# Kernel tuning notes

Hardware: AMD Instinct MI355X
Metric: run time of the kernel (lower is better)

The kernel has to match this reference:

```python
import jax, jax.numpy as jnp
import numpy as np

B, T, E = 4, 2048, 512
H, D = 8, 64            # num_heads, head_size = E // H
HID = H * E             # FFN hidden = num_heads * n_embed (per source)
EPS = 1e-5


def layer_norm(x, g, b):
    mu = jnp.mean(x, axis=-1, keepdims=True)
    var = jnp.var(x, axis=-1, keepdims=True)
    return (x - mu) * jax.lax.rsqrt(var + EPS) * g + b


def setup_inputs() -> dict:
    key = jax.random.key(0)
    ks = jax.random.split(key, 12)
    s_e = 1.0 / np.sqrt(E)
    s_hd = 1.0 / np.sqrt(H * D)
    s_hid = 1.0 / np.sqrt(HID)
    return {
        "x": jax.random.normal(ks[0], (B, T, E), jnp.float32),
        "Wq": jax.random.normal(ks[1], (H, E, D), jnp.float32) * s_e,
        "Wk": jax.random.normal(ks[2], (H, E, D), jnp.float32) * s_e,
        "Wv": jax.random.normal(ks[3], (H, E, D), jnp.float32) * s_e,
        "Wo": jax.random.normal(ks[4], (H * D, E), jnp.float32) * s_hd,
        "bo": jnp.zeros((E,), jnp.float32),
        "W1": jax.random.normal(ks[5], (E, HID), jnp.float32) * s_e,
        "b1": jnp.zeros((HID,), jnp.float32),
        "W2": jax.random.normal(ks[6], (HID, E), jnp.float32) * s_hid,
        "b2": jnp.zeros((E,), jnp.float32),
        "g1": jnp.ones((E,), jnp.float32),
        "be1": jnp.zeros((E,), jnp.float32),
        "g2": jnp.ones((E,), jnp.float32),
        "be2": jnp.zeros((E,), jnp.float32),
    }


def reference(x, Wq, Wk, Wv, Wo, bo, W1, b1, W2, b2, g1, be1, g2, be2):
    # pre-LN decoder block (layer_norm_first=True path)
    xn = layer_norm(x, g1, be1)

    # multi-head causal attention; NOTE: scale is T**-0.5 per the source code
    q = jnp.einsum('bte,hed->bhtd', xn, Wq)
    k = jnp.einsum('bte,hed->bhtd', xn, Wk)
    v = jnp.einsum('bte,hed->bhtd', xn, Wv)
    scores = jnp.einsum('bhtd,bhsd->bhts', q, k) * (T ** -0.5)
    causal = jnp.tril(jnp.ones((T, T), bool))
    scores = jnp.where(causal, scores, -jnp.inf)
    attn = jax.nn.softmax(scores, axis=-1)
    o = jnp.einsum('bhts,bhsd->bhtd', attn, v)           # [B,H,T,D]
    o = o.transpose(0, 2, 1, 3).reshape(B, T, H * D)      # concat heads
    mha = o @ Wo + bo

    x = xn + mha
    xn2 = layer_norm(x, g2, be2)
    ffn = jax.nn.relu(xn2 @ W1 + b1) @ W2 + b2
    return xn2 + ffn
```

## Files before the change

### kernel.cpp

```cpp
#include <hip/hip_runtime.h>
#include <hip/hip_bf16.h>
#include <math.h>

#define Bsz 4
#define Tt 2048
#define Ee 512
#define Hh 8
#define Dd 64
#define HIDs 4096
#define Mrows (Bsz * Tt)

typedef __attribute__((ext_vector_type(8))) short short8;
typedef __attribute__((ext_vector_type(4))) float f32x4;
typedef __attribute__((ext_vector_type(16))) float f32x16;

#define AS1 __attribute__((address_space(1)))
#define AS3 __attribute__((address_space(3)))

__device__ __forceinline__ unsigned short f2bfu(float f) {
    unsigned u = __float_as_uint(f);
    return (unsigned short)((u + 0x7fffu + ((u >> 16) & 1u)) >> 16);
}
__device__ __forceinline__ unsigned short truncbf(float f) {
    return (unsigned short)(__float_as_uint(f) >> 16);
}

__device__ __forceinline__ void ln_body(const float* __restrict__ x,
        const float* __restrict__ g, const float* __restrict__ b,
        const float* __restrict__ addb,
        float* __restrict__ out_f, __hip_bfloat16* __restrict__ out_bf,
        int row) {
    int tid = threadIdx.x;
    const float* xr = x + (size_t)row * Ee;
    float v0 = xr[tid];
    float v1 = xr[tid + 256];
    float s = v0 + v1;
    float sq = v0 * v0 + v1 * v1;
#pragma unroll
    for (int off = 32; off > 0; off >>= 1) {
        s  += __shfl_xor(s, off, 64);
        sq += __shfl_xor(sq, off, 64);
    }
    __shared__ float ls[4], lq[4];
    int wid = tid >> 6, lane = tid & 63;
    if (lane == 0) { ls[wid] = s; lq[wid] = sq; }
    __syncthreads();
    s  = ls[0] + ls[1] + ls[2] + ls[3];
    sq = lq[0] + lq[1] + lq[2] + lq[3];
    float mean = s * (1.0f / Ee);
    float var  = sq * (1.0f / Ee) - mean * mean;
    float rstd = rsqrtf(var + 1e-5f);
    float o0 = (v0 - mean) * rstd * g[tid]       + b[tid];
    float o1 = (v1 - mean) * rstd * g[tid + 256] + b[tid + 256];
    float* orow = out_f + (size_t)row * Ee;
    orow[tid]       = o0 + addb[tid];
    orow[tid + 256] = o1 + addb[tid + 256];
    __hip_bfloat16* brow = out_bf + (size_t)row * Ee;
    brow[tid]       = __float2bfloat16(o0);
    brow[tid + 256] = __float2bfloat16(o1);
}

__global__ __launch_bounds__(256) void ln_kernel(const float* __restrict__ x,
        const float* __restrict__ g, const float* __restrict__ b,
        const float* __restrict__ addb,
        float* __restrict__ out_f, __hip_bfloat16* __restrict__ out_bf) {
    ln_body(x, g, b, addb, out_f, out_bf, blockIdx.x);
}

__device__ __forceinline__ void tr_tile(const float* __restrict__ in,
        __hip_bfloat16* __restrict__ outp, int R, int C, int c0, int r0) {
    __shared__ float tile[64][65];
    int tc = threadIdx.x & 63, tg = threadIdx.x >> 6;
#pragma unroll
    for (int i = 0; i < 16; ++i) {
        int r = tg * 16 + i;
        tile[r][tc] = in[(size_t)(r0 + r) * C + c0 + tc];
    }
    __syncthreads();
#pragma unroll
    for (int i = 0; i < 16; ++i) {
        int cc = tg * 16 + i;
        outp[(size_t)(c0 + cc) * R + r0 + tc] = __float2bfloat16(tile[tc][cc]);
    }
}
__global__ __launch_bounds__(256) void startup_kernel(
        const float* __restrict__ x, const float* __restrict__ g1,
        const float* __restrict__ be1, const float* __restrict__ bo,
        float* __restrict__ xn, __hip_bfloat16* __restrict__ xn_bf,
        const float* __restrict__ Wq, const float* __restrict__ Wk,
        const float* __restrict__ Wv, const float* __restrict__ Wo,
        const float* __restrict__ W1, const float* __restrict__ W2,
        __hip_bfloat16* __restrict__ bqT, __hip_bfloat16* __restrict__ woT,
        __hip_bfloat16* __restrict__ w1T, __hip_bfloat16* __restrict__ w2T) {
    if (blockIdx.x < Mrows) {
        ln_body(x, g1, be1, bo, xn, xn_bf, blockIdx.x);
        return;
    }
    int blk = blockIdx.x - Mrows;
    if (blk < 192) {
        int p = blk >> 6, h = (blk >> 3) & 7, et = blk & 7;
        const float* W = (p == 0) ? Wq : ((p == 1) ? Wk : Wv);
        float sc = (p == 0) ? 0.022097086912079608f * 1.4426950408889634f : 1.0f;
        __shared__ float tile[64][65];
        int td = threadIdx.x & 63, tg = threadIdx.x >> 6;
#pragma unroll
        for (int i = 0; i < 16; ++i) {
            int e = tg * 16 + i;
            tile[e][td] = W[((size_t)h * Ee + et * 64 + e) * Dd + td] * sc;
        }
        __syncthreads();
#pragma unroll
        for (int i = 0; i < 16; ++i) {
            int d = tg * 16 + i;
            bqT[((size_t)(p * 512 + h * 64 + d)) * Ee + et * 64 + td] =
                __float2bfloat16(tile[td][d]);
        }
    } else if (blk < 256) {
        int t = blk - 192;
        tr_tile(Wo, woT, 512, 512, (t & 7) * 64, (t >> 3) * 64);
    } else if (blk < 768) {
        int t = blk - 256;
        tr_tile(W1, w1T, 512, HIDs, (t & 63) * 64, (t >> 6) * 64);
    } else {
        int t = blk - 768;
        tr_tile(W2, w2T, HIDs, 512, (t & 7) * 64, (t >> 3) * 64);
    }
}

__global__ __launch_bounds__(256) void mfma_gemm(
        const __hip_bfloat16* __restrict__ A, int lda,
        const __hip_bfloat16* __restrict__ B, int ldb,
        __hip_bfloat16* __restrict__ Cb, int ldc, int K, int nx) {
    __shared__ __hip_bfloat16 S[16384];
    __hip_bfloat16* As = S;
    __hip_bfloat16* Bs = S + 8192;
    int tid = threadIdx.x;
    int lane = tid & 63, wave = tid >> 6;
    int wm = wave >> 1, wn = wave & 1;
    int L = blockIdx.x;
    int slots = (int)gridDim.x >> 3;
    int v = (L & 7) * slots + (L >> 3);
    int bx = v % nx, by = v / nx;
    int row0 = by * 128, col0 = bx * 128;
    f32x4 acc[4][4];
#pragma unroll
    for (int i = 0; i < 4; ++i)
#pragma unroll
        for (int j = 0; j < 4; ++j) acc[i][j] = (f32x4){0.f, 0.f, 0.f, 0.f};

    int fr = lane & 15;
    int kq = (lane >> 4) << 3;

    for (int k0 = 0; k0 < K; k0 += 64) {
        __syncthreads();
#pragma unroll
        for (int j = 0; j < 4; ++j) {
            int c  = j * 256 + tid;
            int cb = j * 256 + wave * 64;
            int p  = c >> 9, cp = c & 511;
            int r  = cp >> 2, kg = (cp & 3) << 3;
            int ko = k0 + p * 32 + kg;
            __builtin_amdgcn_global_load_lds(
                (const AS1 void*)(A + (size_t)(row0 + r) * lda + ko),
                (AS3 void*)(As + cb * 8), 16, 0, 0);
            __builtin_amdgcn_global_load_lds(
                (const AS1 void*)(B + (size_t)(col0 + r) * ldb + ko),
                (AS3 void*)(Bs + cb * 8), 16, 0, 0);
        }
        __syncthreads();
#pragma unroll
        for (int ks = 0; ks < 2; ++ks) {
            short8 afr[4], bfr[4];
#pragma unroll
            for (int i = 0; i < 4; ++i) {
                afr[i] = *(const short8*)(As + ks * 4096 + (wm * 64 + i * 16 + fr) * 32 + kq);
                bfr[i] = *(const short8*)(Bs + ks * 4096 + (wn * 64 + i * 16 + fr) * 32 + kq);
            }
#pragma unroll
            for (int i = 0; i < 4; ++i)
#pragma unroll
                for (int j = 0; j < 4; ++j)
                    acc[i][j] = __builtin_amdgcn_mfma_f32_16x16x32_bf16(afr[i], bfr[j], acc[i][j], 0, 0, 0);
        }
    }
    __syncthreads();
    unsigned short* Ew = (unsigned short*)S + wave * 1152;
    const __hip_bfloat16* Er = (const __hip_bfloat16*)Ew;
    int rq = (lane >> 4) << 2;
    int rr = lane >> 2, cb2 = (lane & 3) * 16;
#pragma unroll
    for (int i = 0; i < 4; ++i) {
#pragma unroll
        for (int j = 0; j < 4; ++j)
#pragma unroll
            for (int gi = 0; gi < 4; ++gi)
                Ew[(rq + gi) * 72 + j * 16 + fr] = f2bfu(acc[i][j][gi]);
        uint4 v0 = *(const uint4*)(Er + rr * 72 + cb2);
        uint4 v1 = *(const uint4*)(Er + rr * 72 + cb2 + 8);
        size_t rg = (size_t)(row0 + wm * 64 + i * 16 + rr) * ldc + col0 + wn * 64 + cb2;
        *(uint4*)(Cb + rg)     = v0;
        *(uint4*)(Cb + rg + 8) = v1;
    }
}

__global__ __launch_bounds__(256) void mfma_gemm_n64(
        const __hip_bfloat16* __restrict__ A, int lda,
        const __hip_bfloat16* __restrict__ B, int ldb,
        float* __restrict__ Cf, int ldc, int K, int nx) {
    __shared__ __hip_bfloat16 As[2 * 128 * 32];
    __shared__ __hip_bfloat16 Bs[2 * 64 * 32];
    int tid = threadIdx.x;
    int lane = tid & 63, wave = tid >> 6;
    int L = blockIdx.x;
    int slots = (int)gridDim.x >> 3;
    int v = (L & 7) * slots + (L >> 3);
    int bx = v % nx, by = v / nx;
    int row0 = by * 128, col0 = bx * 64;
    f32x4 acc[2][4];
#pragma unroll
    for (int i = 0; i < 2; ++i)
#pragma unroll
        for (int j = 0; j < 4; ++j) acc[i][j] = (f32x4){0.f, 0.f, 0.f, 0.f};

    int fr = lane & 15;
    int kq = (lane >> 4) << 3;

    for (int k0 = 0; k0 < K; k0 += 64) {
        __syncthreads();
#pragma unroll
        for (int j = 0; j < 4; ++j) {
            int c  = j * 256 + tid;
            int cb = j * 256 + wave * 64;
            int p  = c >> 9, cp = c & 511;
            int r  = cp >> 2, kg = (cp & 3) << 3;
            __builtin_amdgcn_global_load_lds(
                (const AS1 void*)(A + (size_t)(row0 + r) * lda + k0 + p * 32 + kg),
                (AS3 void*)(As + cb * 8), 16, 0, 0);
        }
#pragma unroll
        for (int j = 0; j < 2; ++j) {
            int c  = j * 256 + tid;
            int cb = j * 256 + wave * 64;
            int p  = c >> 8, cp = c & 255;
            int r  = cp >> 2, kg = (cp & 3) << 3;
            __builtin_amdgcn_global_load_lds(
                (const AS1 void*)(B + (size_t)(col0 + r) * ldb + k0 + p * 32 + kg),
                (AS3 void*)(Bs + cb * 8), 16, 0, 0);
        }
        __syncthreads();
#pragma unroll
        for (int ks = 0; ks < 2; ++ks) {
            short8 afr[2], bfr[4];
#pragma unroll
            for (int i = 0; i < 2; ++i)
                afr[i] = *(const short8*)(As + ks * 4096 + (wave * 32 + i * 16 + fr) * 32 + kq);
#pragma unroll
            for (int j = 0; j < 4; ++j)
                bfr[j] = *(const short8*)(Bs + ks * 2048 + (j * 16 + fr) * 32 + kq);
#pragma unroll
            for (int i = 0; i < 2; ++i)
#pragma unroll
                for (int j = 0; j < 4; ++j)
                    acc[i][j] = __builtin_amdgcn_mfma_f32_16x16x32_bf16(afr[i], bfr[j], acc[i][j], 0, 0, 0);
        }
    }
    int rq = (lane >> 4) << 2;
#pragma unroll
    for (int i = 0; i < 2; ++i)
#pragma unroll
        for (int j = 0; j < 4; ++j)
#pragma unroll
            for (int gidx = 0; gidx < 4; ++gidx) {
                int r = row0 + wave * 32 + i * 16 + rq + gidx;
                int c = col0 + j * 16 + fr;
                Cf[(size_t)r * ldc + c] += acc[i][j][gidx];
            }
}

__global__ __launch_bounds__(256) void mfma_gemm256(
        const __hip_bfloat16* __restrict__ A, int lda,
        const __hip_bfloat16* __restrict__ B, int ldb,
        __hip_bfloat16* __restrict__ Cb, int ldc, int K,
        const float* __restrict__ bias) {
    __shared__ __hip_bfloat16 S[24576];
    __hip_bfloat16* As = S;
    __hip_bfloat16* Bs = S + 16384;
    int tid = threadIdx.x;
    int lane = tid & 63, wave = tid >> 6;
    int L = blockIdx.x;
    int k8 = L & 7, sub = L >> 3;
    int sr = k8 >> 1, sc = k8 & 1;
    int by = sr * 8 + (sub >> 4);
    int bx = sc * 16 + (sub & 15);
    int row0 = by * 256, col0 = bx * 128;
    f32x4 acc[4][8];
#pragma unroll
    for (int i = 0; i < 4; ++i)
#pragma unroll
        for (int j = 0; j < 8; ++j) acc[i][j] = (f32x4){0.f, 0.f, 0.f, 0.f};

    int fr = lane & 15;
    int kq = (lane >> 4) << 3;
    int nsteps = K >> 5;

#define STAGE256(st, buf)                                                     \
    do {                                                                      \
        int ko_ = (st) << 5;                                                  \
        _Pragma("unroll")                                                     \
        for (int j = 0; j < 4; ++j) {                                         \
            int c = j * 256 + tid;                                            \
            int cb = j * 256 + wave * 64;                                     \
            int r = c >> 2, kg = (c & 3) << 3;                                \
            __builtin_amdgcn_global_load_lds(                                 \
                (const AS1 void*)(A + (size_t)(row0 + r) * lda + ko_ + kg),   \
                (AS3 void*)(As + (buf) * 8192 + cb * 8), 16, 0, 0);           \
        }                                                                     \
        _Pragma("unroll")                                                     \
        for (int j = 0; j < 2; ++j) {                                         \
            int c = j * 256 + tid;                                            \
            int cb = j * 256 + wave * 64;                                     \
            int r = c >> 2, kg = (c & 3) << 3;                                \
            __builtin_amdgcn_global_load_lds(                                 \
                (const AS1 void*)(B + (size_t)(col0 + r) * ldb + ko_ + kg),   \
                (AS3 void*)(Bs + (buf) * 4096 + cb * 8), 16, 0, 0);           \
        }                                                                     \
    } while (0)

    STAGE256(0, 0);
    __syncthreads();
    for (int st = 0; st < nsteps; ++st) {
        int buf = st & 1;
        if (st + 1 < nsteps) STAGE256(st + 1, buf ^ 1);
        short8 afr[4], bfr[8];
#pragma unroll
        for (int i = 0; i < 4; ++i)
            afr[i] = *(const short8*)(As + buf * 8192 + (wave * 64 + i * 16 + fr) * 32 + kq);
#pragma unroll
        for (int j = 0; j < 8; ++j)
            bfr[j] = *(const short8*)(Bs + buf * 4096 + (j * 16 + fr) * 32 + kq);
#pragma unroll
        for (int i = 0; i < 4; ++i)
#pragma unroll
            for (int j = 0; j < 8; ++j)
                acc[i][j] = __builtin_amdgcn_mfma_f32_16x16x32_bf16(afr[i], bfr[j], acc[i][j], 0, 0, 0);
        __syncthreads();
    }
#undef STAGE256

    float bv[8];
#pragma unroll
    for (int j = 0; j < 8; ++j) bv[j] = bias[col0 + j * 16 + fr];
    unsigned short* Ew = (unsigned short*)S + wave * 2176;
    const __hip_bfloat16* Er = (const __hip_bfloat16*)Ew;
    int rq = (lane >> 4) << 2;
    int rr = lane >> 2, cb2 = (lane & 3) * 32;
#pragma unroll
    for (int i = 0; i < 4; ++i) {
#pragma unroll
        for (int j = 0; j < 8; ++j)
#pragma unroll
            for (int gi = 0; gi < 4; ++gi) {
                float t = acc[i][j][gi] + bv[j];
                Ew[(rq + gi) * 136 + j * 16 + fr] = f2bfu(t > 0.f ? t : 0.f);
            }
        size_t rg = (size_t)(row0 + wave * 64 + i * 16 + rr) * ldc + col0 + cb2;
#pragma unroll
        for (int u = 0; u < 4; ++u)
            *(uint4*)(Cb + rg + u * 8) = *(const uint4*)(Er + rr * 136 + cb2 + u * 8);
    }
}

__global__ __launch_bounds__(256) void attn_mfma(const __hip_bfloat16* __restrict__ qkvb,
        __hip_bfloat16* __restrict__ ob) {
    __shared__ __hip_bfloat16 KsS[2][64 * 72];
    __shared__ __hip_bfloat16 VtS[2][64 * 72];
    __shared__ __hip_bfloat16 PsS[4 * 32 * 72];
    __hip_bfloat16* Qs = PsS;

    const unsigned short* q16 = (const unsigned short*)qkvb;
    int tid  = threadIdx.x;
    int lane = tid & 63, wave = tid >> 6;
    int l31 = lane & 31, l5 = lane >> 5;
    int blk = blockIdx.x;
    int qb  = 15 - (blk >> 5);
    int bh  = blk & 31;
    int b = bh >> 3, h = bh & 7;
    int base = qb * 128;
    size_t tokbase = (size_t)b * Tt;
    int qoff = h * 64, koff = 512 + h * 64, voff = 1024 + h * 64;

    {
        int q = tid >> 1, dg = (tid & 1) * 32;
        const unsigned short* src = q16 + (tokbase + base + q) * 1536 + qoff + dg;
        uint4 a  = *(const uint4*)src;
        uint4 b4 = *(const uint4*)(src + 8);
        uint4 c4 = *(const uint4*)(src + 16);
        uint4 d4 = *(const uint4*)(src + 24);
        *(uint4*)(Qs + q * 72 + dg)      = a;
        *(uint4*)(Qs + q * 72 + dg + 8)  = b4;
        *(uint4*)(Qs + q * 72 + dg + 16) = c4;
        *(uint4*)(Qs + q * 72 + dg + 24) = d4;
    }
    __syncthreads();
    short8 aq[4];
#pragma unroll
    for (int kd = 0; kd < 4; ++kd)
        aq[kd] = *(const short8*)(Qs + (wave * 32 + l31) * 72 + kd * 16 + l5 * 8);

    short8 ones;
#pragma unroll
    for (int i = 0; i < 8; ++i) ones[i] = (short)0x3F80;

    f32x16 acc[2], accL;
#pragma unroll
    for (int i = 0; i < 16; ++i) { acc[0][i] = 0.f; acc[1][i] = 0.f; accL[i] = 0.f; }
    __hip_bfloat16* Psw = PsS + wave * (32 * 72);
    unsigned short* Psw16 = (unsigned short*)Psw;

    int s_k = tid >> 2, dg_k = (tid & 3) * 16;
    int sp = (tid & 31) * 2, dg8 = (tid >> 5) * 8;
    uint4 kr0, kr1, va, vb;
    {
        const unsigned short* kp = q16 + (tokbase + s_k) * 1536 + koff + dg_k;
        kr0 = *(const uint4*)kp;
        kr1 = *(const uint4*)(kp + 8);
        const unsigned short* vp = q16 + (tokbase + sp) * 1536 + voff + dg8;
        va = *(const uint4*)vp;
        vb = *(const uint4*)(vp + 1536);
    }

    int tmax = 2 * qb + 1;
    for (int tile = 0; tile <= tmax; ++tile) {
        int buf = tile & 1;
        *(uint4*)(KsS[buf] + s_k * 72 + dg_k)     = kr0;
        *(uint4*)(KsS[buf] + s_k * 72 + dg_k + 8) = kr1;
        {
            unsigned a0[4] = {va.x, va.y, va.z, va.w};
            unsigned b0[4] = {vb.x, vb.y, vb.z, vb.w};
#pragma unroll
            for (int i = 0; i < 4; ++i) {
                unsigned p0 = (a0[i] & 0xffffu) | (b0[i] << 16);
                unsigned p1 = (a0[i] >> 16) | (b0[i] & 0xffff0000u);
                *(unsigned*)(VtS[buf] + (dg8 + 2 * i) * 72 + sp)     = p0;
                *(unsigned*)(VtS[buf] + (dg8 + 2 * i + 1) * 72 + sp) = p1;
            }
        }
        __syncthreads();
        if (tile < tmax) {
            int s1 = (tile + 1) * 64;
            const unsigned short* kp = q16 + (tokbase + s1 + s_k) * 1536 + koff + dg_k;
            kr0 = *(const uint4*)kp;
            kr1 = *(const uint4*)(kp + 8);
            const unsigned short* vp = q16 + (tokbase + s1 + sp) * 1536 + voff + dg8;
            va = *(const uint4*)vp;
            vb = *(const uint4*)(vp + 1536);
        }
        if (tile == tmax && wave < 2) continue;
        f32x16 Sc[2];
#pragma unroll
        for (int i = 0; i < 16; ++i) { Sc[0][i] = 0.f; Sc[1][i] = 0.f; }
#pragma unroll
        for (int st = 0; st < 2; ++st)
#pragma unroll
            for (int kd = 0; kd < 4; ++kd) {
                short8 bk = *(const short8*)(KsS[buf] + (st * 32 + l31) * 72 + kd * 16 + l5 * 8);
                Sc[st] = __builtin_amdgcn_mfma_f32_32x32x16_bf16(aq[kd], bk, Sc[st], 0, 0, 0);
            }
        if (tile >= 2 * qb) {
            int s0t = tile * 64;
            int qrb = base + wave * 32 + 4 * l5;
#pragma unroll
            for (int st = 0; st < 2; ++st) {
                int sg = s0t + st * 32 + l31;
#pragma unroll
                for (int reg = 0; reg < 16; ++reg) {
                    int qr = qrb + (reg & 3) + 8 * (reg >> 2);
                    if (sg > qr) Sc[st][reg] = -1e30f;
                }
            }
        }
#pragma unroll
        for (int st = 0; st < 2; ++st)
#pragma unroll
            for (int reg = 0; reg < 16; ++reg) {
                int pr = (reg & 3) + 8 * (reg >> 2) + 4 * l5;
                Psw16[pr * 72 + st * 32 + l31] =
                    truncbf(__builtin_amdgcn_exp2f(Sc[st][reg]));
            }
#pragma unroll
        for (int ks = 0; ks < 4; ++ks) {
            short8 ap = *(const short8*)(Psw + l31 * 72 + ks * 16 + l5 * 8);
            accL = __builtin_amdgcn_mfma_f32_32x32x16_bf16(ap, ones, accL, 0, 0, 0);
#pragma unroll
            for (int dt = 0; dt < 2; ++dt) {
                short8 bv = *(const short8*)(VtS[buf] + (dt * 32 + l31) * 72 + ks * 16 + l5 * 8);
                acc[dt] = __builtin_amdgcn_mfma_f32_32x32x16_bf16(ap, bv, acc[dt], 0, 0, 0);
            }
        }
    }
#pragma unroll
    for (int reg = 0; reg < 16; ++reg) {
        float rl = 1.0f / accL[reg];
        int qr = base + wave * 32 + (reg & 3) + 8 * (reg >> 2) + 4 * l5;
#pragma unroll
        for (int dt = 0; dt < 2; ++dt)
            ob[(tokbase + qr) * 512 + h * 64 + dt * 32 + l31] =
                __float2bfloat16(acc[dt][reg] * rl);
    }
}

extern "C" void kernel_launch(void* const* d_in, const int* in_sizes, int n_in,
                              void* d_out, int out_size, void* d_ws, size_t ws_size,
                              hipStream_t stream) {
    const float* x   = (const float*)d_in[0];
    const float* Wq  = (const float*)d_in[1];
    const float* Wk  = (const float*)d_in[2];
    const float* Wv  = (const float*)d_in[3];
    const float* Wo  = (const float*)d_in[4];
    const float* bo  = (const float*)d_in[5];
    const float* W1  = (const float*)d_in[6];
    const float* b1  = (const float*)d_in[7];
    const float* W2  = (const float*)d_in[8];
    const float* b2  = (const float*)d_in[9];
    const float* g1  = (const float*)d_in[10];
    const float* be1 = (const float*)d_in[11];
    const float* g2  = (const float*)d_in[12];
    const float* be2 = (const float*)d_in[13];
    float* out = (float*)d_out;

    char* ws = (char*)d_ws;
    __hip_bfloat16* bqT    = (__hip_bfloat16*)(ws);
    __hip_bfloat16* woT    = (__hip_bfloat16*)(ws + 1572864);
    __hip_bfloat16* w1T    = (__hip_bfloat16*)(ws + 2097152);
    __hip_bfloat16* w2T    = (__hip_bfloat16*)(ws + 6291456);
    float*          xn     = (float*)(ws + 10485760);
    __hip_bfloat16* xn_bf  = (__hip_bfloat16*)(ws + 27262976);
    __hip_bfloat16* qkv_bf = (__hip_bfloat16*)(ws + 35651584);
    __hip_bfloat16* o_bf   = (__hip_bfloat16*)(ws + 60817408);
    __hip_bfloat16* h_bf   = (__hip_bfloat16*)(ws + 35651584);

    startup_kernel<<<Mrows + 1280, 256, 0, stream>>>(
        x, g1, be1, bo, xn, xn_bf, Wq, Wk, Wv, Wo, W1, W2, bqT, woT, w1T, w2T);
    mfma_gemm<<<768, 256, 0, stream>>>(
        xn_bf, 512, bqT, 512, qkv_bf, 1536, 512, 12);
    attn_mfma<<<Bsz * Hh * (Tt / 128), 256, 0, stream>>>(qkv_bf, o_bf);
    mfma_gemm_n64<<<512, 256, 0, stream>>>(
        o_bf, 512, woT, 512, xn, 512, 512, 8);
    ln_kernel<<<Mrows, 256, 0, stream>>>(xn, g2, be2, b2, out, xn_bf);
    mfma_gemm256<<<1024, 256, 0, stream>>>(
        xn_bf, 512, w1T, 512, h_bf, HIDs, 512, b1);
    mfma_gemm_n64<<<512, 256, 0, stream>>>(
        h_bf, HIDs, w2T, HIDs, out, 512, HIDs, 8);
}
```

Measured before the change: 340.7 us.

## Rewrite FFN1 GEMM as 256x256 tile, 8-wave, four-phase pipelined kernel

Replaces the 256x128 FFN up-projection GEMM with a 256x256 tile kernel using 512 threads (8 waves in a 2x4 layout), a K-step of 64 and XOR-swizzled LDS to avoid bank conflicts. Each K iteration is split into four quarter-phases, with loads for the next tile issued between barriers, explicit vmcnt waits and raised wave priority around the MFMA bursts. The grid is remapped across 8 XCD-interleaved slots. It uses 128KB of LDS and many accumulator registers, which limits occupancy, and the hand-written waitcnt and barrier schedule is fragile.

```diff
diff --git a/kernel.cpp b/kernel.cpp
--- a/kernel.cpp
+++ b/kernel.cpp
@@ -277,96 +277,196 @@
             }
 }
 
-__global__ __launch_bounds__(256) void mfma_gemm256(
+__device__ __forceinline__ short8 ld_frag(const __hip_bfloat16* base, int r, int slot) {
+    return *(const short8*)(base + r * 64 + ((slot ^ (r & 7)) << 3));
+}
+
+__global__ __launch_bounds__(512, 2) void gemm256_8ph(
         const __hip_bfloat16* __restrict__ A, int lda,
         const __hip_bfloat16* __restrict__ B, int ldb,
         __hip_bfloat16* __restrict__ Cb, int ldc, int K,
-        const float* __restrict__ bias) {
-    __shared__ __hip_bfloat16 S[24576];
-    __hip_bfloat16* As = S;
-    __hip_bfloat16* Bs = S + 16384;
+        const float* __restrict__ bias, int nx) {
+    __shared__ __hip_bfloat16 S[65536];
+    __hip_bfloat16* Asb = S;
+    __hip_bfloat16* Bsb = S + 32768;
     int tid = threadIdx.x;
     int lane = tid & 63, wave = tid >> 6;
+    int wm = wave >> 2, wn = wave & 3;
+    int fr = lane & 15, l5 = lane >> 4;
     int L = blockIdx.x;
-    int k8 = L & 7, sub = L >> 3;
-    int sr = k8 >> 1, sc = k8 & 1;
-    int by = sr * 8 + (sub >> 4);
-    int bx = sc * 16 + (sub & 15);
-    int row0 = by * 256, col0 = bx * 128;
-    f32x4 acc[4][8];
-#pragma unroll
-    for (int i = 0; i < 4; ++i)
-#pragma unroll
-        for (int j = 0; j < 8; ++j) acc[i][j] = (f32x4){0.f, 0.f, 0.f, 0.f};
-
-    int fr = lane & 15;
-    int kq = (lane >> 4) << 3;
-    int nsteps = K >> 5;
-
-#define STAGE256(st, buf)                                                     \
+    int slots = (int)gridDim.x >> 3;
+    int v = (L & 7) * slots + (L >> 3);
+    int bx = v % nx, by = v / nx;
+    int row0 = by * 256, col0 = bx * 256;
+    int T = K >> 6;
+
+    f32x4 acc[8][4];
+#pragma unroll
+    for (int i = 0; i < 8; ++i)
+#pragma unroll
+        for (int j = 0; j < 4; ++j) acc[i][j] = (f32x4){0.f, 0.f, 0.f, 0.f};
+
+#define STAGE_A(tt, hh, bb)                                                   \
     do {                                                                      \
-        int ko_ = (st) << 5;                                                  \
-        _Pragma("unroll")                                                     \
-        for (int j = 0; j < 4; ++j) {                                         \
-            int c = j * 256 + tid;                                            \
-            int cb = j * 256 + wave * 64;                                     \
-            int r = c >> 2, kg = (c & 3) << 3;                                \
-            __builtin_amdgcn_global_load_lds(                                 \
-                (const AS1 void*)(A + (size_t)(row0 + r) * lda + ko_ + kg),   \
-                (AS3 void*)(As + (buf) * 8192 + cb * 8), 16, 0, 0);           \
-        }                                                                     \
         _Pragma("unroll")                                                     \
         for (int j = 0; j < 2; ++j) {                                         \
-            int c = j * 256 + tid;                                            \
-            int cb = j * 256 + wave * 64;                                     \
-            int r = c >> 2, kg = (c & 3) << 3;                                \
+            int c = j * 512 + tid;                                            \
+            int r = c >> 3;                                                   \
+            int sl = (c & 7) ^ (r & 7);                                       \
+            int cb = j * 512 + wave * 64;                                     \
+            int grow = row0 + ((r >> 6) << 7) + (hh) * 64 + (r & 63);         \
             __builtin_amdgcn_global_load_lds(                                 \
-                (const AS1 void*)(B + (size_t)(col0 + r) * ldb + ko_ + kg),   \
-                (AS3 void*)(Bs + (buf) * 4096 + cb * 8), 16, 0, 0);           \
+                (const AS1 void*)(A + (size_t)grow * lda + (tt) * 64 + sl * 8), \
+                (AS3 void*)(Asb + (bb) * 16384 + (hh) * 8192 + cb * 8), 16, 0, 0); \
         }                                                                     \
     } while (0)
-
-    STAGE256(0, 0);
+#define STAGE_B(tt, hh, bb)                                                   \
+    do {                                                                      \
+        _Pragma("unroll")                                                     \
+        for (int j = 0; j < 2; ++j) {                                         \
+            int c = j * 512 + tid;                                            \
+            int r = c >> 3;                                                   \
+            int sl = (c & 7) ^ (r & 7);                                       \
+            int cb = j * 512 + wave * 64;                                     \
+            int gcol = col0 + ((r >> 5) << 6) + (hh) * 32 + (r & 31);         \
+            __builtin_amdgcn_global_load_lds(                                 \
+                (const AS1 void*)(B + (size_t)gcol * ldb + (tt) * 64 + sl * 8), \
+                (AS3 void*)(Bsb + (bb) * 16384 + (hh) * 8192 + cb * 8), 16, 0, 0); \
+        }                                                                     \
+    } while (0)
+
+    STAGE_A(0, 0, 0);
+    STAGE_B(0, 0, 0);
+    STAGE_B(0, 1, 0);
+    STAGE_A(0, 1, 0);
+
+    short8 a[4][2], b[2][2][2];
+    for (int t = 0; t < T; ++t) {
+        int buf = t & 1, nb = buf ^ 1;
+        int tn = (t + 1 < T) ? t + 1 : 0;
+        const __hip_bfloat16* Ab0 = Asb + buf * 16384;
+        const __hip_bfloat16* Ab1 = Ab0 + 8192;
+        const __hip_bfloat16* Bb0 = Bsb + buf * 16384;
+        const __hip_bfloat16* Bb1 = Bb0 + 8192;
+
+        STAGE_A(tn, 0, nb);
+        asm volatile("s_waitcnt vmcnt(6)" ::: "memory");
+        __builtin_amdgcn_s_barrier();
+        asm volatile("" ::: "memory");
+#pragma unroll
+        for (int i = 0; i < 4; ++i)
+#pragma unroll
+            for (int ks = 0; ks < 2; ++ks)
+                a[i][ks] = ld_frag(Ab0, wm * 64 + i * 16 + fr, ks * 4 + l5);
+#pragma unroll
+        for (int jj = 0; jj < 2; ++jj)
+#pragma unroll
+            for (int ks = 0; ks < 2; ++ks)
+                b[0][jj][ks] = ld_frag(Bb0, wn * 32 + jj * 16 + fr, ks * 4 + l5);
+        __builtin_amdgcn_s_setprio(1);
+#pragma unroll
+        for (int i = 0; i < 4; ++i)
+#pragma unroll
+            for (int jj = 0; jj < 2; ++jj)
+#pragma unroll
+                for (int ks = 0; ks < 2; ++ks)
+                    acc[i][jj] = __builtin_amdgcn_mfma_f32_16x16x32_bf16(
+                        a[i][ks], b[0][jj][ks], acc[i][jj], 0, 0, 0);
+        __builtin_amdgcn_s_setprio(0);
+        asm volatile("" ::: "memory");
+        __builtin_amdgcn_s_barrier();
+        asm volatile("" ::: "memory");
+
+        STAGE_B(tn, 0, nb);
+        asm volatile("s_waitcnt vmcnt(6)" ::: "memory");
+        __builtin_amdgcn_s_barrier();
+        asm volatile("" ::: "memory");
+#pragma unroll
+        for (int jj = 0; jj < 2; ++jj)
+#pragma unroll
+            for (int ks = 0; ks < 2; ++ks)
+                b[1][jj][ks] = ld_frag(Bb1, wn * 32 + jj * 16 + fr, ks * 4 + l5);
+        __builtin_amdgcn_s_setprio(1);
+#pragma unroll
+        for (int i = 0; i < 4; ++i)
+#pragma unroll
+            for (int jj = 0; jj < 2; ++jj)
+#pragma unroll
+                for (int ks = 0; ks < 2; ++ks)
+                    acc[i][2 + jj] = __builtin_amdgcn_mfma_f32_16x16x32_bf16(
+                        a[i][ks], b[1][jj][ks], acc[i][2 + jj], 0, 0, 0);
+        __builtin_amdgcn_s_setprio(0);
+        asm volatile("" ::: "memory");
+        __builtin_amdgcn_s_barrier();
+        asm volatile("" ::: "memory");
+
+        STAGE_B(tn, 1, nb);
+        asm volatile("s_waitcnt vmcnt(6)" ::: "memory");
+        __builtin_amdgcn_s_barrier();
+        asm volatile("" ::: "memory");
+#pragma unroll
+        for (int i = 0; i < 4; ++i)
+#pragma unroll
+            for (int ks = 0; ks < 2; ++ks)
+                a[i][ks] = ld_frag(Ab1, wm * 64 + i * 16 + fr, ks * 4 + l5);
+        __builtin_amdgcn_s_setprio(1);
+#pragma unroll
+        for (int i = 0; i < 4; ++i)
+#pragma unroll
+            for (int jj = 0; jj < 2; ++jj)
+#pragma unroll
+                for (int ks = 0; ks < 2; ++ks)
+                    acc[4 + i][2 + jj] = __builtin_amdgcn_mfma_f32_16x16x32_bf16(
+                        a[i][ks], b[1][jj][ks], acc[4 + i][2 + jj], 0, 0, 0);
+        __builtin_amdgcn_s_setprio(0);
+        asm volatile("" ::: "memory");
+        __builtin_amdgcn_s_barrier();
+        asm volatile("" ::: "memory");
+
+        STAGE_A(tn, 1, nb);
+        asm volatile("" ::: "memory");
+        __builtin_amdgcn_s_barrier();
+        asm volatile("" ::: "memory");
+        __builtin_amdgcn_s_setprio(1);
+#pragma unroll
+        for (int i = 0; i < 4; ++i)
+#pragma unroll
+            for (int jj = 0; jj < 2; ++jj)
+#pragma unroll
+                for (int ks = 0; ks < 2; ++ks)
+                    acc[4 + i][jj] = __builtin_amdgcn_mfma_f32_16x16x32_bf16(
+                        a[i][ks], b[0][jj][ks], acc[4 + i][jj], 0, 0, 0);
+        __builtin_amdgcn_s_setprio(0);
+        asm volatile("" ::: "memory");
+        __builtin_amdgcn_s_barrier();
+        asm volatile("" ::: "memory");
+    }
+#undef STAGE_A
+#undef STAGE_B
+
     __syncthreads();
-    for (int st = 0; st < nsteps; ++st) {
-        int buf = st & 1;
-        if (st + 1 < nsteps) STAGE256(st + 1, buf ^ 1);
-        short8 afr[4], bfr[8];
-#pragma unroll
-        for (int i = 0; i < 4; ++i)
-            afr[i] = *(const short8*)(As + buf * 8192 + (wave * 64 + i * 16 + fr) * 32 + kq);
-#pragma unroll
-        for (int j = 0; j < 8; ++j)
-            bfr[j] = *(const short8*)(Bs + buf * 4096 + (j * 16 + fr) * 32 + kq);
-#pragma unroll
-        for (int i = 0; i < 4; ++i)
-#pragma unroll
-            for (int j = 0; j < 8; ++j)
-                acc[i][j] = __builtin_amdgcn_mfma_f32_16x16x32_bf16(afr[i], bfr[j], acc[i][j], 0, 0, 0);
-        __syncthreads();
-    }
-#undef STAGE256
-
-    float bv[8];
-#pragma unroll
-    for (int j = 0; j < 8; ++j) bv[j] = bias[col0 + j * 16 + fr];
-    unsigned short* Ew = (unsigned short*)S + wave * 2176;
+    float bvv[4];
+#pragma unroll
+    for (int nj = 0; nj < 4; ++nj) bvv[nj] = bias[col0 + wn * 64 + nj * 16 + fr];
+    unsigned short* Ew = (unsigned short*)S + wave * 1152;
     const __hip_bfloat16* Er = (const __hip_bfloat16*)Ew;
-    int rq = (lane >> 4) << 2;
-    int rr = lane >> 2, cb2 = (lane & 3) * 32;
-#pragma unroll
-    for (int i = 0; i < 4; ++i) {
-#pragma unroll
-        for (int j = 0; j < 8; ++j)
+    int rq = l5 << 2;
+    int rr = lane >> 2, cb2 = (lane & 3) * 16;
+#pragma unroll
+    for (int mi = 0; mi < 8; ++mi) {
+#pragma unroll
+        for (int nj = 0; nj < 4; ++nj)
 #pragma unroll
             for (int gi = 0; gi < 4; ++gi) {
-                float t = acc[i][j][gi] + bv[j];
-                Ew[(rq + gi) * 136 + j * 16 + fr] = f2bfu(t > 0.f ? t : 0.f);
-            }
-        size_t rg = (size_t)(row0 + wave * 64 + i * 16 + rr) * ldc + col0 + cb2;
-#pragma unroll
-        for (int u = 0; u < 4; ++u)
-            *(uint4*)(Cb + rg + u * 8) = *(const uint4*)(Er + rr * 136 + cb2 + u * 8);
+                float tv = acc[mi][nj][gi] + bvv[nj];
+                Ew[(rq + gi) * 72 + nj * 16 + fr] = f2bfu(tv > 0.f ? tv : 0.f);
+            }
+        uint4 v0 = *(const uint4*)(Er + rr * 72 + cb2);
+        uint4 v1 = *(const uint4*)(Er + rr * 72 + cb2 + 8);
+        size_t rg = (size_t)(row0 + wm * 128 + mi * 16 + rr) * ldc
+                    + col0 + wn * 64 + cb2;
+        *(uint4*)(Cb + rg)     = v0;
+        *(uint4*)(Cb + rg + 8) = v1;
     }
 }
 
@@ -547,8 +647,8 @@
     mfma_gemm_n64<<<512, 256, 0, stream>>>(
         o_bf, 512, woT, 512, xn, 512, 512, 8);
     ln_kernel<<<Mrows, 256, 0, stream>>>(xn, g2, be2, b2, out, xn_bf);
-    mfma_gemm256<<<1024, 256, 0, stream>>>(
-        xn_bf, 512, w1T, 512, h_bf, HIDs, 512, b1);
+    gemm256_8ph<<<512, 512, 0, stream>>>(
+        xn_bf, 512, w1T, 512, h_bf, HIDs, 512, b1, 16);
     mfma_gemm_n64<<<512, 256, 0, stream>>>(
         h_bf, HIDs, w2T, HIDs, out, 512, HIDs, 8);
 }
```

Measured after the change: 308.4 us. 9.5% less time.
